# Performance work log

Measured on AMD Instinct MI355X. Metric: run time of the kernel, lower is better.

## Reference

```python
import jax, jax.numpy as jnp
import numpy as np

TEMPERATURE = 0.5
EPS = 1e-12  # F.normalize eps


def setup_inputs() -> dict:
    key = jax.random.key(0)
    z = jax.random.normal(key, (2048, 8, 256), dtype=jnp.float32)
    return {"z": z}


def reference(z):
    B, D = z.shape[0], z.shape[1]
    z = z.reshape(B, D, -1)  # [B, D, F]
    # F.normalize along features
    norm = jnp.linalg.norm(z, axis=-1, keepdims=True)
    zn = z / jnp.maximum(norm, EPS)

    # Positive term: per sample b, sim among D views -> [B, D, D], off-diagonal sum
    sim_pos = jnp.exp(jnp.einsum('bdf,bef->bde', zn, zn) / TEMPERATURE)
    eye_d = jnp.eye(D, dtype=bool)
    pos = jnp.sum(jnp.where(eye_d[None], 0.0, sim_pos), axis=(1, 2))  # [B]

    # Negative term: per view d, sim among B samples -> [D, B, B], row-wise off-diag mean, summed over views
    sim_neg = jnp.exp(jnp.einsum('bdf,cdf->dbc', zn, zn) / TEMPERATURE)
    eye_b = jnp.eye(B, dtype=bool)
    neg = jnp.sum(jnp.where(eye_b[None], 0.0, sim_neg), axis=-1) / (B - 1)  # [D, B]
    neg = jnp.sum(neg, axis=0)  # [B]

    logits = pos / (pos + neg)  # [B]
    # torch CrossEntropyLoss(reduction='sum') with 1-D input [C] and float target ones(C):
    # loss = -sum_c target_c * log_softmax(logits)_c = -sum(log_softmax(logits))
    error = -jnp.sum(jax.nn.log_softmax(logits))
    return error / B
```

## Files before the change

kernel.cpp:

```cpp
#include <hip/hip_runtime.h>
#include <hip/hip_bf16.h>

#define B_N 2048
#define D_V 8
#define F_D 256
#define TILE 128
#define BC 32
#define LSTR 264

#define SCALE_F 1.69864364f

#if defined(__has_builtin)
#  if __has_builtin(__builtin_amdgcn_exp2f)
#    define EXP2F(x) __builtin_amdgcn_exp2f(x)
#  else
#    define EXP2F(x) exp2f(x)
#  endif
#else
#  define EXP2F(x) exp2f(x)
#endif

typedef __attribute__((ext_vector_type(8))) short short8;
typedef __attribute__((ext_vector_type(4))) float floatx4;

__device__ inline unsigned short f2bf(float f) {
    __hip_bfloat16 h = __float2bfloat16(f);
    return *reinterpret_cast<unsigned short*>(&h);
}

__device__ inline float wave_reduce_sum(float v) {
    #pragma unroll
    for (int off = 1; off < 64; off <<= 1)
        v += __shfl_xor(v, off, 64);
    return v;
}

__device__ inline float wave_reduce_max(float v) {
    #pragma unroll
    for (int off = 1; off < 64; off <<= 1)
        v = fmaxf(v, __shfl_xor(v, off, 64));
    return v;
}

__global__ __launch_bounds__(256)
void np_kernel(const float* __restrict__ z, unsigned short* __restrict__ zn,
               float* __restrict__ ns8, float* __restrict__ pos) {
    __shared__ __align__(16) unsigned short Zs[32 * LSTR];
    int tid = threadIdx.x;
    int gid = blockIdx.x * 256 + tid;
    if (gid < D_V * B_N) ns8[gid] = 0.0f;

    int w = tid >> 6, lane = tid & 63;
    int b = blockIdx.x * 4 + w;
    #pragma unroll
    for (int k = 0; k < 8; k++) {
        const float4 v = ((const float4*)(z + ((size_t)b * 8 + k) * F_D))[lane];
        float ss = v.x * v.x + v.y * v.y + v.z * v.z + v.w * v.w;
        ss = wave_reduce_sum(ss);
        float inv = SCALE_F / fmaxf(sqrtf(ss), 1e-12f);
        ushort4 o;
        o.x = f2bf(v.x * inv);
        o.y = f2bf(v.y * inv);
        o.z = f2bf(v.z * inv);
        o.w = f2bf(v.w * inv);
        ((ushort4*)(zn + (size_t)k * (B_N * F_D) + (size_t)b * F_D))[lane] = o;
        *(ushort4*)(&Zs[(w * 8 + k) * LSTR + lane * 4]) = o;
    }
    __syncthreads();

    if (w < 2) {
        int q = lane >> 4, li = lane & 15;
        int lr = (w * 2 + (li >> 3)) * 8 + (li & 7);
        short8 a[8];
        #pragma unroll
        for (int kk = 0; kk < 8; kk++)
            a[kk] = *(const short8*)(&Zs[lr * LSTR + kk * 32 + q * 8]);
        floatx4 acc = {0.f, 0.f, 0.f, 0.f};
        #pragma unroll
        for (int kk = 0; kk < 8; kk++)
            acc = __builtin_amdgcn_mfma_f32_16x16x32_bf16(a[kk], a[kk], acc, 0, 0, 0);
        float p0 = 0.f, p1 = 0.f;
        #pragma unroll
        for (int r = 0; r < 4; r++) {
            int row = q * 4 + r, col = li;
            bool same_sample = (row >> 3) == (col >> 3);
            if (same_sample && row != col) {
                float e = EXP2F(acc[r]);
                if (row < 8) p0 += e; else p1 += e;
            }
        }
        p0 = wave_reduce_sum(p0);
        p1 = wave_reduce_sum(p1);
        if (lane == 0) {
            int s0 = blockIdx.x * 4 + w * 2;
            pos[s0] = p0;
            pos[s0 + 1] = p1;
        }
    }
}

__global__ __launch_bounds__(256, 4)
void neg_kernel(const unsigned short* __restrict__ zn,
                float* __restrict__ ns8) {
    __shared__ __align__(16) unsigned short Bs[2][BC * LSTR];
    const int bid = blockIdx.x;
    const int d = bid & 7;
    int trem = bid >> 3;
    int i = 0;
    while (trem >= 16 - i) { trem -= 16 - i; ++i; }
    const int j = i + trem;
    const bool diag = (i == j);
    const unsigned short* Z = zn + (size_t)d * (B_N * F_D);
    int tid = threadIdx.x, w = tid >> 6, lane = tid & 63;
    int q = lane >> 4, li = lane & 15;
    int r0 = i * TILE + w * 32;
    const int jc = j * TILE;

    short8 a[2][8];
    #pragma unroll
    for (int s = 0; s < 2; s++)
        #pragma unroll
        for (int kk = 0; kk < 8; kk++)
            a[s][kk] = *(const short8*)(Z + (size_t)(r0 + s * 16 + li) * F_D + kk * 32 + q * 8);

    short8 breg[4];
    #pragma unroll
    for (int it = 0; it < 4; ++it) {
        int idx = it * 256 + tid;
        int row = idx >> 5, kc = idx & 31;
        breg[it] = *(const short8*)(Z + (size_t)(jc + row) * F_D + kc * 8);
    }
    #pragma unroll
    for (int it = 0; it < 4; ++it) {
        int idx = it * 256 + tid;
        int row = idx >> 5, kc = idx & 31;
        *(short8*)(&Bs[0][row * LSTR + kc * 8]) = breg[it];
    }
    #pragma unroll
    for (int it = 0; it < 4; ++it) {
        int idx = it * 256 + tid;
        int row = idx >> 5, kc = idx & 31;
        breg[it] = *(const short8*)(Z + (size_t)(jc + BC + row) * F_D + kc * 8);
    }

    float rs[2][4];
    #pragma unroll
    for (int s = 0; s < 2; s++)
        #pragma unroll
        for (int r = 0; r < 4; r++) rs[s][r] = 0.f;
    float cacc[2] = {0.f, 0.f};

    __syncthreads();

    #pragma unroll
    for (int st = 0; st < 4; ++st) {
        #pragma unroll
        for (int ct = 0; ct < 2; ++ct) {
            const unsigned short* bp = &Bs[st & 1][(ct * 16 + li) * LSTR + q * 8];
            floatx4 acc[2];
            acc[0] = (floatx4){0.f, 0.f, 0.f, 0.f};
            acc[1] = (floatx4){0.f, 0.f, 0.f, 0.f};
            #pragma unroll
            for (int kk = 0; kk < 8; kk++) {
                short8 bf = *(const short8*)(bp + kk * 32);
                acc[0] = __builtin_amdgcn_mfma_f32_16x16x32_bf16(a[0][kk], bf, acc[0], 0, 0, 0);
                acc[1] = __builtin_amdgcn_mfma_f32_16x16x32_bf16(a[1][kk], bf, acc[1], 0, 0, 0);
            }
            int gcol = jc + st * BC + ct * 16 + li;
            float csum = 0.f;
            #pragma unroll
            for (int s = 0; s < 2; s++) {
                #pragma unroll
                for (int r = 0; r < 4; r++) {
                    float e = EXP2F(acc[s][r]);
                    if (diag) {
                        int grow = r0 + s * 16 + q * 4 + r;
                        if (grow == gcol) e = 0.f;
                    }
                    rs[s][r] += e;
                    csum += e;
                }
            }
            csum += __shfl_xor(csum, 16, 64);
            csum += __shfl_xor(csum, 32, 64);
            const int g = st * 2 + ct;
            if (q == (g & 3)) cacc[g >> 2] += csum;
        }
        if (st < 3) {
            #pragma unroll
            for (int it = 0; it < 4; ++it) {
                int idx = it * 256 + tid;
                int row = idx >> 5, kc = idx & 31;
                *(short8*)(&Bs[(st + 1) & 1][row * LSTR + kc * 8]) = breg[it];
            }
        }
        if (st < 2) {
            #pragma unroll
            for (int it = 0; it < 4; ++it) {
                int idx = it * 256 + tid;
                int row = idx >> 5, kc = idx & 31;
                breg[it] = *(const short8*)(Z + (size_t)(jc + (st + 2) * BC + row) * F_D + kc * 8);
            }
        }
        __syncthreads();
    }

    #pragma unroll
    for (int off = 1; off < 16; off <<= 1)
        #pragma unroll
        for (int s = 0; s < 2; s++)
            #pragma unroll
            for (int r = 0; r < 4; r++)
                rs[s][r] += __shfl_xor(rs[s][r], off, 64);
    {
        float rv = 0.f;
        #pragma unroll
        for (int s = 0; s < 2; s++)
            #pragma unroll
            for (int r = 0; r < 4; r++)
                if (li == s * 4 + r) rv = rs[s][r];
        if (li < 8)
            atomicAdd(&ns8[d * B_N + r0 + (li >> 2) * 16 + q * 4 + (li & 3)], rv);
    }

    if (!diag) {
        atomicAdd(&ns8[d * B_N + jc + q * 16 + li], cacc[0]);
        atomicAdd(&ns8[d * B_N + jc + 64 + q * 16 + li], cacc[1]);
    }
}

__global__ void final_kernel(const float* __restrict__ pos,
                             const float* __restrict__ ns8,
                             float* __restrict__ out) {
    __shared__ float redm[4], reds[4], redl[4];
    int t = threadIdx.x, w = t >> 6, lane = t & 63;
    float vals[8];
    float lmax = -1e30f;
    #pragma unroll
    for (int i = 0; i < 8; i++) {
        int idx = t * 8 + i;
        float nsum = 0.f;
        #pragma unroll
        for (int d = 0; d < D_V; d++) nsum += ns8[d * B_N + idx];
        float p = pos[idx];
        float l = p / (p + nsum * (1.0f / (float)(B_N - 1)));
        vals[i] = l;
        lmax = fmaxf(lmax, l);
    }
    lmax = wave_reduce_max(lmax);
    if (lane == 0) redm[w] = lmax;
    __syncthreads();
    float m = fmaxf(fmaxf(redm[0], redm[1]), fmaxf(redm[2], redm[3]));
    float se = 0.f, sl = 0.f;
    #pragma unroll
    for (int i = 0; i < 8; i++) { se += expf(vals[i] - m); sl += vals[i]; }
    se = wave_reduce_sum(se);
    sl = wave_reduce_sum(sl);
    if (lane == 0) { reds[w] = se; redl[w] = sl; }
    __syncthreads();
    if (t == 0) {
        float S = reds[0] + reds[1] + reds[2] + reds[3];
        float L = redl[0] + redl[1] + redl[2] + redl[3];
        out[0] = m + logf(S) - L * (1.0f / (float)B_N);
    }
}

extern "C" void kernel_launch(void* const* d_in, const int* in_sizes, int n_in,
                              void* d_out, int out_size, void* d_ws, size_t ws_size,
                              hipStream_t stream) {
    const float* z = (const float*)d_in[0];
    float* out = (float*)d_out;
    unsigned short* zn = (unsigned short*)d_ws;
    float* ns8 = (float*)((char*)d_ws + (size_t)D_V * B_N * F_D * 2);
    float* pos = ns8 + D_V * B_N;

    np_kernel<<<dim3(512), 256, 0, stream>>>(z, zn, ns8, pos);
    neg_kernel<<<dim3(136 * 8), 256, 0, stream>>>(zn, ns8);
    final_kernel<<<1, 256, 0, stream>>>(pos, ns8, out);
}
```

Before: 102.9 us.

## Use 512-thread blocks in neg_kernel with 16 rows per wave and single LDS buffer

```diff
diff --git a/kernel.cpp b/kernel.cpp
--- a/kernel.cpp
+++ b/kernel.cpp
@@ -5,7 +5,7 @@
 #define D_V 8
 #define F_D 256
 #define TILE 128
-#define BC 32
+#define BC 64
 #define LSTR 264
 
 #define SCALE_F 1.69864364f
@@ -99,10 +99,10 @@
     }
 }
 
-__global__ __launch_bounds__(256, 4)
+__global__ __launch_bounds__(512)
 void neg_kernel(const unsigned short* __restrict__ zn,
                 float* __restrict__ ns8) {
-    __shared__ __align__(16) unsigned short Bs[2][BC * LSTR];
+    __shared__ __align__(16) unsigned short Bs[BC * LSTR];
     const int bid = blockIdx.x;
     const int d = bid & 7;
     int trem = bid >> 3;
@@ -113,119 +113,99 @@
     const unsigned short* Z = zn + (size_t)d * (B_N * F_D);
     int tid = threadIdx.x, w = tid >> 6, lane = tid & 63;
     int q = lane >> 4, li = lane & 15;
-    int r0 = i * TILE + w * 32;
+    int r0 = i * TILE + w * 16;
     const int jc = j * TILE;
 
-    short8 a[2][8];
-    #pragma unroll
-    for (int s = 0; s < 2; s++)
-        #pragma unroll
-        for (int kk = 0; kk < 8; kk++)
-            a[s][kk] = *(const short8*)(Z + (size_t)(r0 + s * 16 + li) * F_D + kk * 32 + q * 8);
+    short8 a[8];
+    #pragma unroll
+    for (int kk = 0; kk < 8; kk++)
+        a[kk] = *(const short8*)(Z + (size_t)(r0 + li) * F_D + kk * 32 + q * 8);
 
     short8 breg[4];
     #pragma unroll
     for (int it = 0; it < 4; ++it) {
-        int idx = it * 256 + tid;
+        int idx = it * 512 + tid;
         int row = idx >> 5, kc = idx & 31;
         breg[it] = *(const short8*)(Z + (size_t)(jc + row) * F_D + kc * 8);
     }
     #pragma unroll
     for (int it = 0; it < 4; ++it) {
-        int idx = it * 256 + tid;
+        int idx = it * 512 + tid;
         int row = idx >> 5, kc = idx & 31;
-        *(short8*)(&Bs[0][row * LSTR + kc * 8]) = breg[it];
+        *(short8*)(&Bs[row * LSTR + kc * 8]) = breg[it];
     }
     #pragma unroll
     for (int it = 0; it < 4; ++it) {
-        int idx = it * 256 + tid;
+        int idx = it * 512 + tid;
         int row = idx >> 5, kc = idx & 31;
         breg[it] = *(const short8*)(Z + (size_t)(jc + BC + row) * F_D + kc * 8);
     }
 
-    float rs[2][4];
-    #pragma unroll
-    for (int s = 0; s < 2; s++)
-        #pragma unroll
-        for (int r = 0; r < 4; r++) rs[s][r] = 0.f;
-    float cacc[2] = {0.f, 0.f};
-
-    __syncthreads();
-
-    #pragma unroll
-    for (int st = 0; st < 4; ++st) {
-        #pragma unroll
-        for (int ct = 0; ct < 2; ++ct) {
-            const unsigned short* bp = &Bs[st & 1][(ct * 16 + li) * LSTR + q * 8];
-            floatx4 acc[2];
-            acc[0] = (floatx4){0.f, 0.f, 0.f, 0.f};
-            acc[1] = (floatx4){0.f, 0.f, 0.f, 0.f};
+    float rs[4] = {0.f, 0.f, 0.f, 0.f};
+    float cs[8];
+
+    __syncthreads();
+
+    #pragma unroll
+    for (int stage = 0; stage < 2; ++stage) {
+        #pragma unroll
+        for (int ct = 0; ct < 4; ++ct) {
+            const unsigned short* bp = &Bs[(ct * 16 + li) * LSTR + q * 8];
+            floatx4 acc = {0.f, 0.f, 0.f, 0.f};
             #pragma unroll
             for (int kk = 0; kk < 8; kk++) {
                 short8 bf = *(const short8*)(bp + kk * 32);
-                acc[0] = __builtin_amdgcn_mfma_f32_16x16x32_bf16(a[0][kk], bf, acc[0], 0, 0, 0);
-                acc[1] = __builtin_amdgcn_mfma_f32_16x16x32_bf16(a[1][kk], bf, acc[1], 0, 0, 0);
-            }
-            int gcol = jc + st * BC + ct * 16 + li;
+                acc = __builtin_amdgcn_mfma_f32_16x16x32_bf16(a[kk], bf, acc, 0, 0, 0);
+            }
+            int gcol = jc + stage * BC + ct * 16 + li;
             float csum = 0.f;
             #pragma unroll
-            for (int s = 0; s < 2; s++) {
-                #pragma unroll
-                for (int r = 0; r < 4; r++) {
-                    float e = EXP2F(acc[s][r]);
-                    if (diag) {
-                        int grow = r0 + s * 16 + q * 4 + r;
-                        if (grow == gcol) e = 0.f;
-                    }
-                    rs[s][r] += e;
-                    csum += e;
+            for (int r = 0; r < 4; r++) {
+                float e = EXP2F(acc[r]);
+                if (diag) {
+                    int grow = r0 + q * 4 + r;
+                    if (grow == gcol) e = 0.f;
                 }
+                rs[r] += e;
+                csum += e;
             }
             csum += __shfl_xor(csum, 16, 64);
             csum += __shfl_xor(csum, 32, 64);
-            const int g = st * 2 + ct;
-            if (q == (g & 3)) cacc[g >> 2] += csum;
-        }
-        if (st < 3) {
+            cs[stage * 4 + ct] = csum;
+        }
+        if (stage == 0) {
+            __syncthreads();
             #pragma unroll
             for (int it = 0; it < 4; ++it) {
-                int idx = it * 256 + tid;
+                int idx = it * 512 + tid;
                 int row = idx >> 5, kc = idx & 31;
-                *(short8*)(&Bs[(st + 1) & 1][row * LSTR + kc * 8]) = breg[it];
-            }
-        }
-        if (st < 2) {
-            #pragma unroll
-            for (int it = 0; it < 4; ++it) {
-                int idx = it * 256 + tid;
-                int row = idx >> 5, kc = idx & 31;
-                breg[it] = *(const short8*)(Z + (size_t)(jc + (st + 2) * BC + row) * F_D + kc * 8);
-            }
-        }
-        __syncthreads();
+                *(short8*)(&Bs[row * LSTR + kc * 8]) = breg[it];
+            }
+            __syncthreads();
+        }
     }
 
     #pragma unroll
     for (int off = 1; off < 16; off <<= 1)
         #pragma unroll
-        for (int s = 0; s < 2; s++)
-            #pragma unroll
-            for (int r = 0; r < 4; r++)
-                rs[s][r] += __shfl_xor(rs[s][r], off, 64);
+        for (int r = 0; r < 4; r++)
+            rs[r] += __shfl_xor(rs[r], off, 64);
     {
         float rv = 0.f;
         #pragma unroll
-        for (int s = 0; s < 2; s++)
-            #pragma unroll
-            for (int r = 0; r < 4; r++)
-                if (li == s * 4 + r) rv = rs[s][r];
-        if (li < 8)
-            atomicAdd(&ns8[d * B_N + r0 + (li >> 2) * 16 + q * 4 + (li & 3)], rv);
+        for (int r = 0; r < 4; r++)
+            if (li == r) rv = rs[r];
+        if (li < 4)
+            atomicAdd(&ns8[d * B_N + r0 + q * 4 + li], rv);
     }
 
     if (!diag) {
-        atomicAdd(&ns8[d * B_N + jc + q * 16 + li], cacc[0]);
-        atomicAdd(&ns8[d * B_N + jc + 64 + q * 16 + li], cacc[1]);
+        float v0 = 0.f, v1 = 0.f;
+        #pragma unroll
+        for (int c = 0; c < 4; c++)
+            if (q == c) { v0 = cs[c]; v1 = cs[c + 4]; }
+        atomicAdd(&ns8[d * B_N + jc + q * 16 + li], v0);
+        atomicAdd(&ns8[d * B_N + jc + 64 + q * 16 + li], v1);
     }
 }
 
@@ -275,6 +255,6 @@
     float* pos = ns8 + D_V * B_N;
 
     np_kernel<<<dim3(512), 256, 0, stream>>>(z, zn, ns8, pos);
-    neg_kernel<<<dim3(136 * 8), 256, 0, stream>>>(zn, ns8);
+    neg_kernel<<<dim3(136 * 8), 512, 0, stream>>>(zn, ns8);
     final_kernel<<<1, 256, 0, stream>>>(pos, ns8, out);
 }
```

New measurement: 86.80 us. 1.19x faster.

## Split neg_kernel into single-wave blocks loading B operands directly from global

Applied to the files above, without the earlier changes.

```diff
diff --git a/kernel.cpp b/kernel.cpp
--- a/kernel.cpp
+++ b/kernel.cpp
@@ -5,7 +5,6 @@
 #define D_V 8
 #define F_D 256
 #define TILE 128
-#define BC 32
 #define LSTR 264
 
 #define SCALE_F 1.69864364f
@@ -99,21 +98,22 @@
     }
 }
 
-__global__ __launch_bounds__(256, 4)
+__global__ __launch_bounds__(64, 3)
 void neg_kernel(const unsigned short* __restrict__ zn,
                 float* __restrict__ ns8) {
-    __shared__ __align__(16) unsigned short Bs[2][BC * LSTR];
     const int bid = blockIdx.x;
     const int d = bid & 7;
-    int trem = bid >> 3;
+    int rest = bid >> 3;
+    const int sub = rest & 3;
+    int trem = rest >> 2;
     int i = 0;
     while (trem >= 16 - i) { trem -= 16 - i; ++i; }
     const int j = i + trem;
     const bool diag = (i == j);
     const unsigned short* Z = zn + (size_t)d * (B_N * F_D);
-    int tid = threadIdx.x, w = tid >> 6, lane = tid & 63;
+    int lane = threadIdx.x & 63;
     int q = lane >> 4, li = lane & 15;
-    int r0 = i * TILE + w * 32;
+    const int r0 = i * TILE + sub * 32;
     const int jc = j * TILE;
 
     short8 a[2][8];
@@ -123,86 +123,46 @@
         for (int kk = 0; kk < 8; kk++)
             a[s][kk] = *(const short8*)(Z + (size_t)(r0 + s * 16 + li) * F_D + kk * 32 + q * 8);
 
-    short8 breg[4];
-    #pragma unroll
-    for (int it = 0; it < 4; ++it) {
-        int idx = it * 256 + tid;
-        int row = idx >> 5, kc = idx & 31;
-        breg[it] = *(const short8*)(Z + (size_t)(jc + row) * F_D + kc * 8);
-    }
-    #pragma unroll
-    for (int it = 0; it < 4; ++it) {
-        int idx = it * 256 + tid;
-        int row = idx >> 5, kc = idx & 31;
-        *(short8*)(&Bs[0][row * LSTR + kc * 8]) = breg[it];
-    }
-    #pragma unroll
-    for (int it = 0; it < 4; ++it) {
-        int idx = it * 256 + tid;
-        int row = idx >> 5, kc = idx & 31;
-        breg[it] = *(const short8*)(Z + (size_t)(jc + BC + row) * F_D + kc * 8);
-    }
-
     float rs[2][4];
     #pragma unroll
     for (int s = 0; s < 2; s++)
         #pragma unroll
         for (int r = 0; r < 4; r++) rs[s][r] = 0.f;
-    float cacc[2] = {0.f, 0.f};
-
-    __syncthreads();
-
-    #pragma unroll
-    for (int st = 0; st < 4; ++st) {
-        #pragma unroll
-        for (int ct = 0; ct < 2; ++ct) {
-            const unsigned short* bp = &Bs[st & 1][(ct * 16 + li) * LSTR + q * 8];
-            floatx4 acc[2];
-            acc[0] = (floatx4){0.f, 0.f, 0.f, 0.f};
-            acc[1] = (floatx4){0.f, 0.f, 0.f, 0.f};
+    float cs[8];
+
+    #pragma unroll
+    for (int ct = 0; ct < 8; ++ct) {
+        const unsigned short* bp = Z + (size_t)(jc + ct * 16 + li) * F_D + q * 8;
+        short8 bf[8];
+        #pragma unroll
+        for (int kk = 0; kk < 8; kk++)
+            bf[kk] = *(const short8*)(bp + kk * 32);
+        floatx4 acc[2];
+        acc[0] = (floatx4){0.f, 0.f, 0.f, 0.f};
+        acc[1] = (floatx4){0.f, 0.f, 0.f, 0.f};
+        #pragma unroll
+        for (int kk = 0; kk < 8; kk++) {
+            acc[0] = __builtin_amdgcn_mfma_f32_16x16x32_bf16(a[0][kk], bf[kk], acc[0], 0, 0, 0);
+            acc[1] = __builtin_amdgcn_mfma_f32_16x16x32_bf16(a[1][kk], bf[kk], acc[1], 0, 0, 0);
+        }
+        int gcol = jc + ct * 16 + li;
+        float csum = 0.f;
+        #pragma unroll
+        for (int s = 0; s < 2; s++) {
             #pragma unroll
-            for (int kk = 0; kk < 8; kk++) {
-                short8 bf = *(const short8*)(bp + kk * 32);
-                acc[0] = __builtin_amdgcn_mfma_f32_16x16x32_bf16(a[0][kk], bf, acc[0], 0, 0, 0);
-                acc[1] = __builtin_amdgcn_mfma_f32_16x16x32_bf16(a[1][kk], bf, acc[1], 0, 0, 0);
+            for (int r = 0; r < 4; r++) {
+                float e = EXP2F(acc[s][r]);
+                if (diag) {
+                    int grow = r0 + s * 16 + q * 4 + r;
+                    if (grow == gcol) e = 0.f;
+                }
+                rs[s][r] += e;
+                csum += e;
             }
-            int gcol = jc + st * BC + ct * 16 + li;
-            float csum = 0.f;
-            #pragma unroll
-            for (int s = 0; s < 2; s++) {
-                #pragma unroll
-                for (int r = 0; r < 4; r++) {
-                    float e = EXP2F(acc[s][r]);
-                    if (diag) {
-                        int grow = r0 + s * 16 + q * 4 + r;
-                        if (grow == gcol) e = 0.f;
-                    }
-                    rs[s][r] += e;
-                    csum += e;
-                }
-            }
-            csum += __shfl_xor(csum, 16, 64);
-            csum += __shfl_xor(csum, 32, 64);
-            const int g = st * 2 + ct;
-            if (q == (g & 3)) cacc[g >> 2] += csum;
-        }
-        if (st < 3) {
-            #pragma unroll
-            for (int it = 0; it < 4; ++it) {
-                int idx = it * 256 + tid;
-                int row = idx >> 5, kc = idx & 31;
-                *(short8*)(&Bs[(st + 1) & 1][row * LSTR + kc * 8]) = breg[it];
-            }
-        }
-        if (st < 2) {
-            #pragma unroll
-            for (int it = 0; it < 4; ++it) {
-                int idx = it * 256 + tid;
-                int row = idx >> 5, kc = idx & 31;
-                breg[it] = *(const short8*)(Z + (size_t)(jc + (st + 2) * BC + row) * F_D + kc * 8);
-            }
-        }
-        __syncthreads();
+        }
+        csum += __shfl_xor(csum, 16, 64);
+        csum += __shfl_xor(csum, 32, 64);
+        cs[ct] = csum;
     }
 
     #pragma unroll
@@ -224,8 +184,12 @@
     }
 
     if (!diag) {
-        atomicAdd(&ns8[d * B_N + jc + q * 16 + li], cacc[0]);
-        atomicAdd(&ns8[d * B_N + jc + 64 + q * 16 + li], cacc[1]);
+        float v0 = 0.f, v1 = 0.f;
+        #pragma unroll
+        for (int c = 0; c < 4; c++)
+            if (q == c) { v0 = cs[c]; v1 = cs[c + 4]; }
+        atomicAdd(&ns8[d * B_N + jc + q * 16 + li], v0);
+        atomicAdd(&ns8[d * B_N + jc + 64 + q * 16 + li], v1);
     }
 }
 
@@ -275,6 +239,6 @@
     float* pos = ns8 + D_V * B_N;
 
     np_kernel<<<dim3(512), 256, 0, stream>>>(z, zn, ns8, pos);
-    neg_kernel<<<dim3(136 * 8), 256, 0, stream>>>(zn, ns8);
+    neg_kernel<<<dim3(136 * 4 * 8), 64, 0, stream>>>(zn, ns8);
     final_kernel<<<1, 256, 0, stream>>>(pos, ns8, out);
 }
```

After: 113.4 us. 1.1x slower.
